# Kernel optimization log

Measured on AMD Instinct MI355X. Metric: run time of the kernel, lower is better.

## Reference

```python
import jax, jax.numpy as jnp
import numpy as np

DIM = 1024
NUM_HEADS = 16
HEAD_DIM = DIM // NUM_HEADS


def apply_rotary_embed(x, thetas):
    # x: (..., seq, d), thetas: (seq, d) broadcast over leading dims
    x1, x2 = jnp.split(x, 2, axis=-1)
    x_rot = jnp.concatenate([-x2, x1], axis=-1)
    return x * jnp.cos(thetas) + x_rot * jnp.sin(thetas)


def setup_inputs() -> dict:
    key = jax.random.key(0)
    ks = jax.random.split(key, 8)
    B, Nx, Nc = 4, 1024, 2048
    x = jax.random.normal(ks[0], (B, Nx, DIM), dtype=jnp.float32)
    c = jax.random.normal(ks[1], (B, Nc, DIM), dtype=jnp.float32)
    x_pos_embed = jax.random.normal(ks[2], (Nx, HEAD_DIM), dtype=jnp.float32)
    c_pos_embed = jax.random.normal(ks[3], (Nc, HEAD_DIM), dtype=jnp.float32)
    s = 1.0 / np.sqrt(DIM)
    Wq = jax.random.normal(ks[4], (DIM, DIM), dtype=jnp.float32) * s
    Wkv = jax.random.normal(ks[5], (DIM, 2 * DIM), dtype=jnp.float32) * s
    Wproj = jax.random.normal(ks[6], (DIM, DIM), dtype=jnp.float32) * s
    bproj = jnp.zeros((DIM,), dtype=jnp.float32)
    return {"x": x, "c": c, "x_pos_embed": x_pos_embed, "c_pos_embed": c_pos_embed,
            "Wq": Wq, "Wkv": Wkv, "Wproj": Wproj, "bproj": bproj}


def reference(x, c, x_pos_embed, c_pos_embed, Wq, Wkv, Wproj, bproj):
    B, Nx, D = x.shape
    Nc = c.shape[1]
    H, hd = NUM_HEADS, HEAD_DIM
    # Q projection -> (B, H, Nx, hd)
    q = (x @ Wq).reshape(B, Nx, H, hd).transpose(0, 2, 1, 3)
    q = apply_rotary_embed(q, x_pos_embed)
    # KV projection -> k, v each (B, H, Nc, hd)
    kv = (c @ Wkv).reshape(B, Nc, 2, H, hd).transpose(2, 0, 3, 1, 4)
    k, v = kv[0], kv[1]
    k = apply_rotary_embed(k, c_pos_embed)
    # scaled dot-product attention (dropout p=0 -> identity)
    scale = 1.0 / np.sqrt(hd).astype(np.float32)
    attn = jnp.einsum('bhqd,bhkd->bhqk', q, k) * scale
    attn = jax.nn.softmax(attn, axis=-1)
    out = jnp.einsum('bhqk,bhkd->bhqd', attn, v)
    out = out.transpose(0, 2, 1, 3).reshape(B, Nx, D)
    return out @ Wproj + bproj
```

## Files before the change

### kernel.cpp

```cpp
#include <hip/hip_runtime.h>
#include <math.h>

#define DIMC  1024
#define NHEAD 16
#define HD    64
#define NB    4
#define NX    1024
#define NC    2048
#define KD    1024

typedef _Float16 half_t;
typedef __attribute__((ext_vector_type(8))) _Float16 h8;
typedef __attribute__((ext_vector_type(4))) _Float16 h4;
typedef __attribute__((ext_vector_type(2))) __fp16 fp16x2;
typedef __attribute__((ext_vector_type(4))) float f32x4;

#define QSCALE 0.1803368801111244f
#define NEGM  -8.656170245333781f

__device__ __forceinline__ void gload_lds16(const half_t* g, half_t* l) {
    __builtin_amdgcn_global_load_lds(
        (__attribute__((address_space(1))) void*)(g),
        (__attribute__((address_space(3))) void*)(l), 16, 0, 0);
}

__device__ __forceinline__ void wtile(const float* __restrict__ W,
                                      half_t* __restrict__ Wt, int N, int IMG,
                                      int bx, int by, int t)
{
    __shared__ half_t T[64][72];
    const int k0 = by * 64, n0 = bx * 64;
    const int kr = t >> 2, c0 = (t & 3) << 4;
    const float* src = W + (size_t)(k0 + kr) * N + n0 + c0;
#pragma unroll
    for (int j = 0; j < 16; j += 4) {
        float4 v = *(const float4*)(src + j);
        T[c0 + j + 0][kr] = (half_t)v.x;
        T[c0 + j + 1][kr] = (half_t)v.y;
        T[c0 + j + 2][kr] = (half_t)v.z;
        T[c0 + j + 3][kr] = (half_t)v.w;
    }
    __syncthreads();
    const int nr = t >> 2, kc = (t & 3) << 4;
    if (!IMG) {
        half_t* dst = Wt + (size_t)(n0 + nr) * KD + k0 + kc;
        *(int4*)dst       = *(const int4*)&T[nr][kc];
        *(int4*)(dst + 8) = *(const int4*)&T[nr][kc + 8];
    } else {
        const int n = n0 + nr;
        const int ntile = n >> 8, rr = n & 255;
        const int s0 = kc >> 3;
        half_t* base = Wt + ((size_t)(ntile * 16 + by) * 256 + rr) * 64;
        *(int4*)(base + ((s0 ^ (rr & 7)) << 3))       = *(const int4*)&T[nr][kc];
        *(int4*)(base + (((s0 + 1) ^ (rr & 7)) << 3)) = *(const int4*)&T[nr][kc + 8];
    }
}

__global__ __launch_bounds__(256) void prep(
    const float* __restrict__ x, half_t* __restrict__ xh,
    const float* __restrict__ c, half_t* __restrict__ ch,
    const float* __restrict__ xpe, const float* __restrict__ cpe,
    float* __restrict__ xct, float* __restrict__ xst,
    float* __restrict__ cct, float* __restrict__ cst,
    const float* __restrict__ Wq,  half_t* __restrict__ Wqt,
    const float* __restrict__ Wkv, half_t* __restrict__ Wkt,
    const float* __restrict__ Wp,  half_t* __restrict__ Wpt)
{
    const int bid = blockIdx.x, t = threadIdx.x;
    if (bid < 1024) {
        if (bid < 256)      wtile(Wq,  Wqt, DIMC, 0,     bid & 15,         bid >> 4,         t);
        else if (bid < 768) wtile(Wkv, Wkt, 2 * DIMC, 1, (bid - 256) & 31, (bid - 256) >> 5, t);
        else                wtile(Wp,  Wpt, DIMC, 0,     (bid - 768) & 15, (bid - 768) >> 4, t);
    } else if (bid < 7168) {
        const int nx = NB * NX * DIMC;
        const int i = ((bid - 1024) * 256 + t) * 8;
        const float* s;
        h8 o;
        if (i < nx) {
            s = x + i;
            float4 a = *(const float4*)(s);
            float4 b = *(const float4*)(s + 4);
            o[0] = (half_t)a.x; o[1] = (half_t)a.y; o[2] = (half_t)a.z; o[3] = (half_t)a.w;
            o[4] = (half_t)b.x; o[5] = (half_t)b.y; o[6] = (half_t)b.z; o[7] = (half_t)b.w;
            *(h8*)(xh + i) = o;
        } else {
            const int j = i - nx;
            s = c + j;
            float4 a = *(const float4*)(s);
            float4 b = *(const float4*)(s + 4);
            o[0] = (half_t)a.x; o[1] = (half_t)a.y; o[2] = (half_t)a.z; o[3] = (half_t)a.w;
            o[4] = (half_t)b.x; o[5] = (half_t)b.y; o[6] = (half_t)b.z; o[7] = (half_t)b.w;
            const int R = j >> 10, k = j & 1023;
            const int mt = R >> 8, r = R & 255, kt = k >> 6, sl = (k & 63) >> 3;
            *(h8*)(ch + ((size_t)(mt * 16 + kt) * 256 + r) * 64 + ((sl ^ (r & 7)) << 3)) = o;
        }
    } else {
        const int i = (bid - 7168) * 256 + t;
        if (i < NX * HD) {
            const float th = xpe[i];
            xct[i] = cosf(th); xst[i] = sinf(th);
        } else {
            const int j = i - NX * HD;
            const float th = cpe[j];
            cct[j] = cosf(th); cst[j] = sinf(th);
        }
    }
}

template <int MODE, int BN>
__global__ __launch_bounds__(256) void hgemm(
    const half_t* __restrict__ Ag, const half_t* __restrict__ Bt,
    const float* __restrict__ ct, const float* __restrict__ st,
    const float* __restrict__ bias,
    void* __restrict__ out0, void* __restrict__ out1)
{
    constexpr int MI = (BN == 128) ? 4 : 2;
    constexpr int BLOADS = BN / 32;
    __shared__ half_t As[2][8192];
    __shared__ half_t Bs[2][BN * 64];

    const int tid = threadIdx.x;
    const int w = tid >> 6, lane = tid & 63;
    const int lr = lane & 15, lg = lane >> 4;
    const int wrOff = (BN == 128) ? (w >> 1) * 64 : w * 32;
    const int wcOff = (BN == 128) ? (w & 1) * 64 : 0;

    int lin = (int)blockIdx.x;
    lin = (lin & 7) * ((int)gridDim.x >> 3) + (lin >> 3);
    const int m0 = (lin >> 4) * 128, n0 = (lin & 15) * BN;

    f32x4 acc[MI][4];
#pragma unroll
    for (int i = 0; i < MI; ++i)
#pragma unroll
        for (int j = 0; j < 4; ++j) acc[i][j] = f32x4{0.f, 0.f, 0.f, 0.f};

    size_t gA[4], gB[BLOADS];
    int loff[4];
#pragma unroll
    for (int c = 0; c < 4; ++c) {
        const int L = c * 4096 + w * 1024 + lane * 16;
        const int row = L >> 7;
        const int ss = ((L >> 4) & 7) ^ (row & 7);
        gA[c] = (size_t)(m0 + row) * KD + ss * 8;
        if (c < BLOADS) gB[c] = (size_t)(n0 + row) * KD + ss * 8;
        loff[c] = c * 2048 + w * 512;
    }

#define HSTAGE(buf, kk) do {                                               \
        _Pragma("unroll")                                                  \
        for (int c = 0; c < 4; ++c) {                                      \
            gload_lds16(Ag + gA[c] + (kk) * 64, &As[buf][loff[c]]);        \
            if (c < BLOADS) gload_lds16(Bt + gB[c] + (kk) * 64, &Bs[buf][loff[c]]); \
        }                                                                  \
    } while (0)

    HSTAGE(0, 0);
    asm volatile("s_waitcnt vmcnt(0)" ::: "memory");
    __builtin_amdgcn_s_barrier();
    __builtin_amdgcn_sched_barrier(0);

    for (int k = 0; k < KD / 64; ++k) {
        const int cb = k & 1;
        if (k + 1 < KD / 64) {
            HSTAGE(cb ^ 1, k + 1);
            if constexpr (BLOADS == 4)
                asm volatile("s_waitcnt vmcnt(8)" ::: "memory");
            else
                asm volatile("s_waitcnt vmcnt(6)" ::: "memory");
        } else {
            asm volatile("s_waitcnt vmcnt(0)" ::: "memory");
        }
        __builtin_amdgcn_s_barrier();
        __builtin_amdgcn_sched_barrier(0);

        __builtin_amdgcn_s_setprio(1);
#pragma unroll
        for (int kc = 0; kc < 2; ++kc) {
            h8 af[MI], bf[4];
#pragma unroll
            for (int mi = 0; mi < MI; ++mi) {
                const int r = wrOff + mi * 16 + lr;
                af[mi] = *(const h8*)&As[cb][r * 64 + (((kc * 4 + lg) ^ (r & 7)) << 3)];
            }
#pragma unroll
            for (int ni = 0; ni < 4; ++ni) {
                const int r = wcOff + ni * 16 + lr;
                bf[ni] = *(const h8*)&Bs[cb][r * 64 + (((kc * 4 + lg) ^ (r & 7)) << 3)];
            }
#pragma unroll
            for (int mi = 0; mi < MI; ++mi)
#pragma unroll
                for (int ni = 0; ni < 4; ++ni)
                    acc[mi][ni] = __builtin_amdgcn_mfma_f32_16x16x32_f16(
                        af[mi], bf[ni], acc[mi][ni], 0, 0, 0);
        }
        __builtin_amdgcn_s_setprio(0);

        __builtin_amdgcn_s_barrier();
        __builtin_amdgcn_sched_barrier(0);
    }
#undef HSTAGE

    if (MODE == 2) {
        float* o = (float*)out0;
#pragma unroll
        for (int ni = 0; ni < 4; ++ni) {
            const int col = n0 + ni * 16 + lr;
            const float bv = bias[col];
#pragma unroll
            for (int mi = 0; mi < MI; ++mi)
#pragma unroll
                for (int r = 0; r < 4; ++r) {
                    const int row = m0 + wrOff + mi * 16 + lg * 4 + r;
                    o[(size_t)row * DIMC + col] = acc[mi][ni][r] + bv;
                }
        }
        return;
    }

    if (MODE == 0) {
        half_t* Qw = (half_t*)out0;
        const int h = n0 >> 6;
#pragma unroll
        for (int mi = 0; mi < MI; ++mi)
#pragma unroll
            for (int r = 0; r < 4; ++r) {
                const int row = m0 + wrOff + mi * 16 + lg * 4 + r;
                const int bb = row >> 10, nn = row & (NX - 1);
                const float* cr = ct + nn * HD;
                const float* sr = st + nn * HD;
                half_t* op = Qw + (((size_t)(bb * NHEAD + h)) * NX + nn) * HD;
#pragma unroll
                for (int ni = 0; ni < 4; ++ni) {
                    const int d = ni * 16 + lr;
                    const float val = acc[mi][ni][r];
                    const float pv  = acc[mi][ni ^ 2][r];
                    op[d] = (half_t)((val * cr[d] + (ni < 2 ? -pv : pv) * sr[d]) * QSCALE);
                }
            }
    }
}

__global__ __launch_bounds__(512, 2) void hgemm_kv(
    const half_t* __restrict__ Aimg, const half_t* __restrict__ Bimg,
    const float* __restrict__ ct, const float* __restrict__ st,
    half_t* __restrict__ Kw, half_t* __restrict__ Vw)
{
    __shared__ half_t lds[65536];

    const int tid = threadIdx.x;
    const int w = tid >> 6, lane = tid & 63;
    const int lr = lane & 15, lg = lane >> 4;
    const int wr = w >> 2, wc = w & 3;
    const int wrOff = wr * 128, wcOff = wc * 64;

    int lin = (int)blockIdx.x;
    lin = (lin & 7) * 32 + (lin >> 3);
    const int mt = lin >> 3, nt = lin & 7;
    const int m0 = mt * 256, n0 = nt * 256;

    const half_t* Ablk = Aimg + (size_t)mt * 262144;
    const half_t* Bblk = Bimg + (size_t)nt * 262144;
    const int so2 = w * 512 + lane * 8;

    f32x4 acc[8][4];
#pragma unroll
    for (int i = 0; i < 8; ++i)
#pragma unroll
        for (int j = 0; j < 4; ++j) acc[i][j] = f32x4{0.f, 0.f, 0.f, 0.f};
    h8 af[2][2];
    h8 bf[4][2];

#define ISSUEH(SRC, DSTOFF) do {                                     \
        gload_lds16((SRC) + so2,        &lds[(DSTOFF) + w * 512]);   \
        gload_lds16((SRC) + 4096 + so2, &lds[(DSTOFF) + 4096 + w * 512]); \
    } while (0)

#define PHASE(MI0, AOFF, BOFF, READBF, STG, GATE) do {               \
        _Pragma("unroll")                                            \
        for (int kc = 0; kc < 2; ++kc)                               \
        _Pragma("unroll")                                            \
        for (int d = 0; d < 2; ++d) {                                \
            const int r_ = wrOff + ((MI0) + d) * 16 + lr;            \
            af[d][kc] = *(const h8*)&lds[(AOFF) + r_ * 64 + (((kc * 4 + lg) ^ (r_ & 7)) << 3)]; \
        }                                                            \
        if (READBF) {                                                \
            _Pragma("unroll")                                        \
            for (int ni = 0; ni < 4; ++ni)                           \
            _Pragma("unroll")                                        \
            for (int kc = 0; kc < 2; ++kc) {                         \
                const int rb = wcOff + ni * 16 + lr;                 \
                bf[ni][kc] = *(const h8*)&lds[(BOFF) + rb * 64 + (((kc * 4 + lg) ^ (rb & 7)) << 3)]; \
            }                                                        \
        }                                                            \
        STG;                                                         \
        __builtin_amdgcn_sched_barrier(0);                           \
        __builtin_amdgcn_s_barrier();                                \
        __builtin_amdgcn_s_setprio(1);                               \
        _Pragma("unroll")                                            \
        for (int d = 0; d < 2; ++d)                                  \
        _Pragma("unroll")                                            \
        for (int ni = 0; ni < 4; ++ni)                               \
        _Pragma("unroll")                                            \
        for (int kc = 0; kc < 2; ++kc)                               \
            acc[(MI0) + d][ni] = __builtin_amdgcn_mfma_f32_16x16x32_f16( \
                af[d][kc], bf[ni][kc], acc[(MI0) + d][ni], 0, 0, 0); \
        __builtin_amdgcn_s_setprio(0);                               \
        GATE;                                                        \
        __builtin_amdgcn_s_barrier();                                \
    } while (0)

#define GATE4 asm volatile("s_waitcnt vmcnt(4)" ::: "memory")
#define GATE0 asm volatile("s_waitcnt vmcnt(0)" ::: "memory")
#define NOG   ((void)0)

    ISSUEH(Ablk, 0);          ISSUEH(Ablk + 8192, 8192);
    ISSUEH(Bblk, 32768);      ISSUEH(Bblk + 8192, 32768 + 8192);
    __builtin_amdgcn_sched_barrier(0);
    ISSUEH(Bblk + 16384, 49152); ISSUEH(Bblk + 16384 + 8192, 49152 + 8192);
    asm volatile("s_waitcnt vmcnt(4)" ::: "memory");
    __builtin_amdgcn_s_barrier();

    for (int i = 0; i < 7; ++i) {
        const half_t* An1 = Ablk + (size_t)(2 * i + 1) * 16384;
        const half_t* An2 = Ablk + (size_t)(2 * i + 2) * 16384;
        const half_t* Bn2 = Bblk + (size_t)(2 * i + 2) * 16384;
        const half_t* Bn3 = Bblk + (size_t)(2 * i + 3) * 16384;
        PHASE(0, 0,     32768, true,  ISSUEH(An1, 16384),               NOG);
        PHASE(2, 0,     32768, false, ISSUEH(An1 + 8192, 16384 + 8192), NOG);
        PHASE(4, 0,     32768, false, ISSUEH(Bn2, 32768),               NOG);
        PHASE(6, 0,     32768, false, ISSUEH(Bn2 + 8192, 32768 + 8192), GATE4);
        PHASE(0, 16384, 49152, true,  ISSUEH(An2, 0),                   NOG);
        PHASE(2, 16384, 49152, false, ISSUEH(An2 + 8192, 8192),         NOG);
        PHASE(4, 16384, 49152, false, ISSUEH(Bn3, 49152),               NOG);
        PHASE(6, 16384, 49152, false, ISSUEH(Bn3 + 8192, 49152 + 8192), GATE4);
    }
    {
        const half_t* A15 = Ablk + (size_t)15 * 16384;
        PHASE(0, 0,     32768, true,  ISSUEH(A15, 16384),               NOG);
        PHASE(2, 0,     32768, false, ISSUEH(A15 + 8192, 16384 + 8192), NOG);
        PHASE(4, 0,     32768, false, NOG,                              NOG);
        PHASE(6, 0,     32768, false, NOG,                              GATE0);
        PHASE(0, 16384, 49152, true,  NOG,                              NOG);
        PHASE(2, 16384, 49152, false, NOG,                              NOG);
        PHASE(4, 16384, 49152, false, NOG,                              NOG);
        PHASE(6, 16384, 49152, false, NOG,                              NOG);
    }
#undef PHASE
#undef ISSUEH
#undef GATE4
#undef GATE0
#undef NOG

    const bool isK = (n0 < DIMC);
    const int h = ((n0 & (DIMC - 1)) >> 6) + wc;
#pragma unroll
    for (int mi = 0; mi < 8; ++mi)
#pragma unroll
        for (int r = 0; r < 4; ++r) {
            const int row = m0 + wrOff + mi * 16 + lg * 4 + r;
            const int bb = row >> 11, nn = row & (NC - 1);
            const int tt = nn >> 6, rr = nn & 63;
            const size_t tbase = ((size_t)(bb * NHEAD + h) * 32 + tt) * 4096;
            const float* cr = ct + nn * HD;
            const float* sr = st + nn * HD;
#pragma unroll
            for (int ni = 0; ni < 4; ++ni) {
                const int d = ni * 16 + lr;
                const float val = acc[mi][ni][r];
                if (isK) {
                    const float pv = acc[mi][ni ^ 2][r];
                    Kw[tbase + rr * 64 + ((((d >> 3) ^ (rr & 7)) << 3) | (d & 7))] =
                        (half_t)(val * cr[d] + (ni < 2 ? -pv : pv) * sr[d]);
                } else {
                    Vw[tbase + d * 64 + ((((rr >> 3) ^ (d & 7)) << 3) | (rr & 7))] =
                        (half_t)val;
                }
            }
        }
}

__global__ __launch_bounds__(512) void attn_mfma(
    const half_t* __restrict__ Q, const half_t* __restrict__ Kg,
    const half_t* __restrict__ Vg,
    float* __restrict__ Opart, float* __restrict__ Lpart)
{
    __shared__ half_t Ks[2][4096];
    __shared__ half_t Vs[2][4096];
    __shared__ half_t Ps[8192];

    const int tid = threadIdx.x;
    const int w = tid >> 6, lane = tid & 63;
    const int lr = lane & 15, lg = lane >> 4;
    const int e7 = lr & 7;

    const int inner = (int)blockIdx.x & 511;
    const int kvh = (int)blockIdx.x >> 9;
    const int sid = (inner & 7) * 64 + (inner >> 3);
    const int bh = sid >> 3;
    const int q0 = (sid & 7) * 128;

    const half_t* qbase = Q + ((size_t)bh * NX + q0 + w * 16 + lr) * HD + lg * 8;
    const h8 qf0 = *(const h8*)(qbase);
    const h8 qf1 = *(const h8*)(qbase + 32);

    f32x4 acc[4];
#pragma unroll
    for (int i = 0; i < 4; ++i) acc[i] = f32x4{0.f, 0.f, 0.f, 0.f};
    f32x4 accl = {0.f, 0.f, 0.f, 0.f};

    h8 vone;
#pragma unroll
    for (int i = 0; i < 8; ++i) vone[i] = (half_t)(lr == 0 ? 1.0f : 0.0f);

    const half_t* Kt = Kg + (size_t)bh * 32 * 4096;
    const half_t* Vt = Vg + (size_t)bh * 32 * 4096;
    const int so = tid * 8;
    const int t0 = kvh * 16, t1 = t0 + 16;

#define STAGE(bi, t) do {                                           \
        gload_lds16(Kt + (size_t)(t) * 4096 + so, &Ks[bi][so]);     \
        gload_lds16(Vt + (size_t)(t) * 4096 + so, &Vs[bi][so]);     \
    } while (0)

    STAGE(0, t0);
    asm volatile("s_waitcnt vmcnt(0)" ::: "memory");
    __builtin_amdgcn_s_barrier();
    __builtin_amdgcn_sched_barrier(0);

    const int rowq = w * 16 + lr;

    for (int t = t0; t < t1; ++t) {
        const int cur = t & 1;
        if (t + 1 < t1) {
            STAGE(cur ^ 1, t + 1);
            asm volatile("s_waitcnt vmcnt(2)" ::: "memory");
        } else {
            asm volatile("s_waitcnt vmcnt(0)" ::: "memory");
        }
        __builtin_amdgcn_s_barrier();
        __builtin_amdgcn_sched_barrier(0);

        f32x4 sc[4];
        __builtin_amdgcn_s_setprio(1);
#pragma unroll
        for (int cb = 0; cb < 4; ++cb) {
            const int r = cb * 16 + lr;
            const h8 kf0 = *(const h8*)&Ks[cur][r * 64 + ((lg ^ e7) << 3)];
            const h8 kf1 = *(const h8*)&Ks[cur][r * 64 + (((4 + lg) ^ e7) << 3)];
            f32x4 a = {NEGM, NEGM, NEGM, NEGM};
            a = __builtin_amdgcn_mfma_f32_16x16x32_f16(kf0, qf0, a, 0, 0, 0);
            a = __builtin_amdgcn_mfma_f32_16x16x32_f16(kf1, qf1, a, 0, 0, 0);
            sc[cb] = a;
        }
        __builtin_amdgcn_s_setprio(0);

#pragma unroll
        for (int cb = 0; cb < 4; ++cb) {
            fp16x2 a01 = __builtin_amdgcn_cvt_pkrtz(exp2f(sc[cb][0]), exp2f(sc[cb][1]));
            fp16x2 a23 = __builtin_amdgcn_cvt_pkrtz(exp2f(sc[cb][2]), exp2f(sc[cb][3]));
            union { h4 h; uint2 u; } pw;
            pw.u.x = *(unsigned int*)&a01;
            pw.u.y = *(unsigned int*)&a23;
            const int s = cb * 2 + (lg >> 1);
            *(h4*)&Ps[rowq * 64 + ((s ^ e7) << 3) + (lg & 1) * 4] = pw.h;
        }

        const h8 pf0 = *(const h8*)&Ps[rowq * 64 + ((lg ^ e7) << 3)];
        const h8 pf1 = *(const h8*)&Ps[rowq * 64 + (((4 + lg) ^ e7) << 3)];
        __builtin_amdgcn_s_setprio(1);
#pragma unroll
        for (int db = 0; db < 4; ++db) {
            const int rd = db * 16 + lr;
            const h8 vf0 = *(const h8*)&Vs[cur][rd * 64 + ((lg ^ e7) << 3)];
            const h8 vf1 = *(const h8*)&Vs[cur][rd * 64 + (((4 + lg) ^ e7) << 3)];
            acc[db] = __builtin_amdgcn_mfma_f32_16x16x32_f16(pf0, vf0, acc[db], 0, 0, 0);
            acc[db] = __builtin_amdgcn_mfma_f32_16x16x32_f16(pf1, vf1, acc[db], 0, 0, 0);
        }
        accl = __builtin_amdgcn_mfma_f32_16x16x32_f16(pf0, vone, accl, 0, 0, 0);
        accl = __builtin_amdgcn_mfma_f32_16x16x32_f16(pf1, vone, accl, 0, 0, 0);
        __builtin_amdgcn_s_setprio(0);

        __builtin_amdgcn_s_barrier();
        __builtin_amdgcn_sched_barrier(0);
    }
#undef STAGE

    const int qblk = (q0 >> 6) + (w >> 2);
    const int slot = (bh * 16 + qblk) * 2 + kvh;
    float* Po = Opart + (size_t)slot * 4096;
    const int qr = (w & 3) * 16;
#pragma unroll
    for (int db = 0; db < 4; ++db)
#pragma unroll
        for (int r = 0; r < 4; ++r)
            Po[(qr + lg * 4 + r) * 64 + db * 16 + lr] = acc[db][r];
    if (lr == 0) {
#pragma unroll
        for (int r = 0; r < 4; ++r)
            Lpart[(size_t)slot * 64 + qr + lg * 4 + r] = accl[r];
    }
}

__global__ __launch_bounds__(256) void combine(
    const float* __restrict__ Opart, const float* __restrict__ Lpart,
    half_t* __restrict__ Ow)
{
    const int pidx = blockIdx.x;
    const int bh = pidx >> 4, qblk = pidx & 15;
    const int b = bh >> 4, h = bh & 15;
    const int t = threadIdx.x;
    const int row = t >> 2;
    const int c0 = (t & 3) << 4;

    const float* P0 = Opart + (size_t)(pidx * 2 + 0) * 4096 + row * 64 + c0;
    const float* P1 = Opart + (size_t)(pidx * 2 + 1) * 4096 + row * 64 + c0;
    const float inv = 1.f / (Lpart[(size_t)(pidx * 2 + 0) * 64 + row] +
                             Lpart[(size_t)(pidx * 2 + 1) * 64 + row]);

    half_t* o = Ow + ((size_t)b * NX + qblk * 64 + row) * DIMC + h * 64 + c0;
#pragma unroll
    for (int j = 0; j < 16; j += 8) {
        float4 a0 = *(const float4*)(P0 + j);
        float4 a1 = *(const float4*)(P0 + j + 4);
        float4 b0 = *(const float4*)(P1 + j);
        float4 b1 = *(const float4*)(P1 + j + 4);
        h8 ov;
        ov[0] = (half_t)((a0.x + b0.x) * inv);
        ov[1] = (half_t)((a0.y + b0.y) * inv);
        ov[2] = (half_t)((a0.z + b0.z) * inv);
        ov[3] = (half_t)((a0.w + b0.w) * inv);
        ov[4] = (half_t)((a1.x + b1.x) * inv);
        ov[5] = (half_t)((a1.y + b1.y) * inv);
        ov[6] = (half_t)((a1.z + b1.z) * inv);
        ov[7] = (half_t)((a1.w + b1.w) * inv);
        *(h8*)(o + j) = ov;
    }
}

extern "C" void kernel_launch(void* const* d_in, const int* in_sizes, int n_in,
                              void* d_out, int out_size, void* d_ws, size_t ws_size,
                              hipStream_t stream)
{
    const float* x     = (const float*)d_in[0];
    const float* c     = (const float*)d_in[1];
    const float* xpe   = (const float*)d_in[2];
    const float* cpe   = (const float*)d_in[3];
    const float* Wq    = (const float*)d_in[4];
    const float* Wkv   = (const float*)d_in[5];
    const float* Wproj = (const float*)d_in[6];
    const float* bproj = (const float*)d_in[7];

    char* wsb = (char*)d_ws;
    half_t* xh  = (half_t*)(wsb);
    half_t* ch  = (half_t*)(wsb + ((size_t)8  << 20));
    half_t* Wqt = (half_t*)(wsb + ((size_t)24 << 20));
    half_t* Wkt = (half_t*)(wsb + ((size_t)26 << 20));
    half_t* Kw  = (half_t*)(wsb + ((size_t)32 << 20));
    half_t* Vw  = (half_t*)(wsb + ((size_t)48 << 20));
    half_t* Ow  = (half_t*)(wsb + ((size_t)64 << 20));
    float*  xct = (float*)(wsb + ((size_t)72 << 20));
    float*  xst = (float*)(wsb + ((size_t)72 << 20) + (256u << 10));
    float*  cct = (float*)(wsb + ((size_t)72 << 20) + (512u << 10));
    float*  cst = (float*)(wsb + ((size_t)72 << 20) + (1024u << 10));
    half_t* Wpt = (half_t*)(wsb + ((size_t)74 << 20));
    float*  Lpart = (float*)(wsb + ((size_t)76 << 20));
    float*  Opart = (float*)(wsb);
    half_t* Qw  = (half_t*)d_out;

    prep<<<7936, 256, 0, stream>>>(x, xh, c, ch, xpe, cpe,
                                   xct, xst, cct, cst,
                                   Wq, Wqt, Wkv, Wkt, Wproj, Wpt);

    hgemm<0, 64><<<512, 256, 0, stream>>>(xh, Wqt, xct, xst, nullptr,
                                          Qw, nullptr);
    hgemm_kv<<<256, 512, 0, stream>>>(ch, Wkt, cct, cst, Kw, Vw);
    attn_mfma<<<1024, 512, 0, stream>>>(Qw, Kw, Vw, Opart, Lpart);
    combine<<<1024, 256, 0, stream>>>(Opart, Lpart, Ow);
    hgemm<2, 64><<<512, 256, 0, stream>>>(Ow, Wpt, nullptr, nullptr, bproj,
                                          (float*)d_out, nullptr);
}
```

Before: 184.8 us.

## Replace LDS round-trip for P tile with cross-lane shuffles in attention

The softmax probabilities were written to a shared-memory P buffer and read back in MFMA operand layout. They are now rearranged in registers with __shfl (ds_bpermute) and a select, and the Ps shared array is removed. That cuts LDS footprint, which together with launch_bounds(512,8) is meant to allow more resident blocks, and avoids an LDS store/load pair per tile. In exchange each tile issues 16 bpermutes, which also go through the LDS crossbar, so the saving may be small.

Measured after the change: 190.8 us. 1.03x slower.

```diff
diff --git a/kernel.cpp b/kernel.cpp
--- a/kernel.cpp
+++ b/kernel.cpp
@@ -381,14 +381,13 @@
         }
 }
 
-__global__ __launch_bounds__(512) void attn_mfma(
+__global__ __launch_bounds__(512, 8) void attn_mfma(
     const half_t* __restrict__ Q, const half_t* __restrict__ Kg,
     const half_t* __restrict__ Vg,
     float* __restrict__ Opart, float* __restrict__ Lpart)
 {
     __shared__ half_t Ks[2][4096];
     __shared__ half_t Vs[2][4096];
-    __shared__ half_t Ps[8192];
 
     const int tid = threadIdx.x;
     const int w = tid >> 6, lane = tid & 63;
@@ -419,6 +418,10 @@
     const int so = tid * 8;
     const int t0 = kvh * 16, t1 = t0 + 16;
 
+    const int src0 = lr + ((lg & 1) << 5);
+    const int src1 = src0 + 16;
+    const bool hi = (lg & 2) != 0;
+
 #define STAGE(bi, t) do {                                           \
         gload_lds16(Kt + (size_t)(t) * 4096 + so, &Ks[bi][so]);     \
         gload_lds16(Vt + (size_t)(t) * 4096 + so, &Vs[bi][so]);     \
@@ -428,8 +431,6 @@
     asm volatile("s_waitcnt vmcnt(0)" ::: "memory");
     __builtin_amdgcn_s_barrier();
     __builtin_amdgcn_sched_barrier(0);
-
-    const int rowq = w * 16 + lr;
 
     for (int t = t0; t < t1; ++t) {
         const int cur = t & 1;
@@ -456,19 +457,35 @@
         }
         __builtin_amdgcn_s_setprio(0);
 
+        unsigned int w0[4], w1[4];
 #pragma unroll
         for (int cb = 0; cb < 4; ++cb) {
             fp16x2 a01 = __builtin_amdgcn_cvt_pkrtz(exp2f(sc[cb][0]), exp2f(sc[cb][1]));
             fp16x2 a23 = __builtin_amdgcn_cvt_pkrtz(exp2f(sc[cb][2]), exp2f(sc[cb][3]));
-            union { h4 h; uint2 u; } pw;
-            pw.u.x = *(unsigned int*)&a01;
-            pw.u.y = *(unsigned int*)&a23;
-            const int s = cb * 2 + (lg >> 1);
-            *(h4*)&Ps[rowq * 64 + ((s ^ e7) << 3) + (lg & 1) * 4] = pw.h;
-        }
-
-        const h8 pf0 = *(const h8*)&Ps[rowq * 64 + ((lg ^ e7) << 3)];
-        const h8 pf1 = *(const h8*)&Ps[rowq * 64 + (((4 + lg) ^ e7) << 3)];
+            w0[cb] = *(unsigned int*)&a01;
+            w1[cb] = *(unsigned int*)&a23;
+        }
+
+        h8 pf0, pf1;
+        {
+            union { h8 h; unsigned int u[4]; } P;
+            unsigned int a, b;
+            a = __shfl((int)w0[0], src0); b = __shfl((int)w0[1], src0); P.u[0] = hi ? b : a;
+            a = __shfl((int)w1[0], src0); b = __shfl((int)w1[1], src0); P.u[1] = hi ? b : a;
+            a = __shfl((int)w0[0], src1); b = __shfl((int)w0[1], src1); P.u[2] = hi ? b : a;
+            a = __shfl((int)w1[0], src1); b = __shfl((int)w1[1], src1); P.u[3] = hi ? b : a;
+            pf0 = P.h;
+        }
+        {
+            union { h8 h; unsigned int u[4]; } P;
+            unsigned int a, b;
+            a = __shfl((int)w0[2], src0); b = __shfl((int)w0[3], src0); P.u[0] = hi ? b : a;
+            a = __shfl((int)w1[2], src0); b = __shfl((int)w1[3], src0); P.u[1] = hi ? b : a;
+            a = __shfl((int)w0[2], src1); b = __shfl((int)w0[3], src1); P.u[2] = hi ? b : a;
+            a = __shfl((int)w1[2], src1); b = __shfl((int)w1[3], src1); P.u[3] = hi ? b : a;
+            pf1 = P.h;
+        }
+
         __builtin_amdgcn_s_setprio(1);
 #pragma unroll
         for (int db = 0; db < 4; ++db) {
```
